# Kernel optimization log

Measured on AMD Instinct MI355X. Metric: run time of the kernel, lower is better.

Reference implementation:

```python
import jax, jax.numpy as jnp
import numpy as np

EPS = 1e-6


def _l2norm_last(x):
    return jnp.linalg.norm(x, axis=-1, keepdims=True)


def rotate_to(src, tgt):
    # rotation trick (vector-quantize-pytorch): Householder-style rotation of src onto tgt direction
    # src, tgt: (b, t, d)
    ns = _l2norm_last(src)
    nt = _l2norm_last(tgt)
    u = src / jnp.maximum(ns, EPS)
    q = tgt / jnp.maximum(nt, EPS)
    w = u + q
    w = jax.lax.stop_gradient(w / jnp.maximum(_l2norm_last(w), EPS))
    e = src
    rotated = (e
               - 2.0 * jnp.sum(e * w, axis=-1, keepdims=True) * w
               + 2.0 * jnp.sum(e * jax.lax.stop_gradient(u), axis=-1, keepdims=True) * q)
    return rotated * jax.lax.stop_gradient(nt / jnp.maximum(ns, EPS))


def _simvq_stage(res, V_i, g_i, b_i, cb_i, commit_w):
    # res: (b, t, D); V_i: (D, cd); g_i, b_i: (D,); cb_i: (cs, cd)
    # weight_norm Conv1d(k=1): W = g * V / ||V||_row
    Wn = g_i[:, None] * V_i / jnp.maximum(jnp.linalg.norm(V_i, axis=1, keepdims=True), 1e-12)
    implicit = cb_i @ Wn.T + b_i  # (cs, D) implicit codebook
    # nearest code via squared-distance argmin (cdist argmin equivalent, no_grad)
    d2 = (jnp.sum(res * res, axis=-1, keepdims=True)
          - 2.0 * jnp.einsum('btd,cd->btc', res, implicit)
          + jnp.sum(implicit * implicit, axis=-1))
    idx = jnp.argmin(d2, axis=-1)  # (b, t) int
    z_q = implicit[idx]  # gather: (b, t, D)
    commit = (jnp.mean((jax.lax.stop_gradient(res) - z_q) ** 2)
              + 0.25 * jnp.mean((res - jax.lax.stop_gradient(z_q)) ** 2))
    z_q = rotate_to(res, z_q)
    return z_q, idx, commit * commit_w


def setup_inputs() -> dict:
    key = jax.random.key(0)
    ks = jax.random.split(key, 5)
    B, D, T = 16, 512, 2048
    N, CS, CD = 9, 1024, 8
    z = jax.random.normal(ks[0], (B, D, T), dtype=jnp.float32)
    V = jax.random.normal(ks[1], (N, D, CD), dtype=jnp.float32)
    g = jax.random.uniform(ks[2], (N, D), dtype=jnp.float32, minval=0.5, maxval=1.5)
    b = jax.random.normal(ks[3], (N, D), dtype=jnp.float32) * 0.01
    CB = jax.random.normal(ks[4], (N, CS, CD), dtype=jnp.float32) * (CD ** -0.5)
    return {"z": z, "V": V, "g": g, "b": b, "CB": CB}


def reference(z, V, g, b, CB):
    # eval-mode ResidualSimVQ forward, all n_codebooks stages
    n_codebooks = V.shape[0]
    res = jnp.transpose(z, (0, 2, 1))  # (b, t, D)
    z_q = jnp.zeros_like(res)
    commitment_loss = jnp.float32(0.0)
    codes = []
    for i in range(n_codebooks):
        z_q_i, idx_i, commit_i = _simvq_stage(res, V[i], g[i], b[i], CB[i], 1.0)
        z_q = z_q + z_q_i
        res = res - z_q_i
        commitment_loss = commitment_loss + commit_i
        codes.append(idx_i)
    z_q = jnp.transpose(z_q, (0, 2, 1))  # (b, D, t)
    codes = jnp.stack(codes, axis=1)  # (b, n_codebooks, t)
    return z_q, codes, commitment_loss
```

## Files before the change

### kernel.cpp

```cpp
#include <hip/hip_runtime.h>


#define NB  16
#define DD  512
#define TT  2048
#define NCB 9
#define CS  1024
#define CD  8
#define KK  9
#define KP  12
#define NBLK (NB * (TT / 16))
#define GAPTHR 0.015f

#define WS_WN_OFF  65536
#define WS_WNF_OFF (WS_WN_OFF  + (size_t)NCB*DD*KK*8)
#define WS_Q_OFF   (WS_WNF_OFF + (size_t)NCB*DD*KP*4)
#define WS_QF_OFF  (WS_Q_OFF   + (size_t)NCB*CS*8)

typedef float vf4 __attribute__((ext_vector_type(4)));

__global__ void k_wn(const float* __restrict__ V, const float* __restrict__ g,
                     const float* __restrict__ bp, double* __restrict__ wn,
                     float* __restrict__ wnf) {
  int gid = blockIdx.x * 256 + threadIdx.x;
  if (gid >= NCB * DD) return;
  int i = gid / DD, d = gid % DD;
  const float* vp = V + (size_t)gid * CD;
  double v[CD], s = 0.0;
#pragma unroll
  for (int k = 0; k < CD; k++) { v[k] = (double)vp[k]; s = fma(v[k], v[k], s); }
  double den = fmax(sqrt(s), 1e-12);
  double gg = (double)g[gid];
  double* row = wn + ((size_t)i * DD + d) * KK;
  float* frow = wnf + ((size_t)i * DD + d) * KP;
#pragma unroll
  for (int k = 0; k < CD; k++) {
    double wv = gg * v[k] / den;
    row[k] = wv;
    frow[k] = (float)wv;
  }
  row[CD] = (double)bp[gid];
  frow[CD] = bp[gid];
  frow[9] = 0.0f; frow[10] = 0.0f; frow[11] = 0.0f;
}

__global__ void k_q(const float* __restrict__ CBp, const float* __restrict__ bp,
                    const double* __restrict__ wn,
                    double* __restrict__ q, float* __restrict__ qf) {
  int wid = blockIdx.x * 4 + (threadIdx.x >> 6);
  int lane = threadIdx.x & 63;
  int i = wid / CS, c = wid % CS;
  const float* cb = CBp + (size_t)(i * CS + c) * CD;
  double cbv[CD];
#pragma unroll
  for (int k = 0; k < CD; k++) cbv[k] = (double)cb[k];
  const double* wnp = wn + (size_t)i * DD * KK;
  const float* bb = bp + (size_t)i * DD;
  double acc = 0.0;
#pragma unroll
  for (int j = 0; j < 8; j++) {
    int d = j * 64 + lane;
    double imp = (double)bb[d];
#pragma unroll
    for (int k = 0; k < CD; k++) imp = fma(cbv[k], wnp[(size_t)d * KK + k], imp);
    acc = fma(imp, imp, acc);
  }
#pragma unroll
  for (int o = 32; o; o >>= 1) acc += __shfl_xor(acc, o, 64);
  if (lane == 0) { q[wid] = acc; qf[wid] = (float)(0.5 * acc); }
}

__launch_bounds__(256, 2)
__global__ void k_main(const float* __restrict__ z, const float* __restrict__ CBp,
                       const double* __restrict__ wn, const float* __restrict__ wnf,
                       const double* __restrict__ qtab, const float* __restrict__ qftab,
                       float* __restrict__ out_zq, float* __restrict__ out_codes,
                       double* __restrict__ partials) {
  __shared__ __align__(16) float tile[DD * 17];
  __shared__ double cbuf[4];

  const int tid = threadIdx.x, lane = tid & 63, w = tid >> 6;
  const int bb = blockIdx.x >> 7, tg = blockIdx.x & 127;
  const int t0 = tg * 16;
  const float* zb = z + (size_t)bb * DD * TT + t0;

#pragma unroll
  for (int m = 0; m < 8; m++) {
    int F = tid + m * 256, d = F >> 2, qq = F & 3;
    const vf4 v = __builtin_nontemporal_load((const vf4*)(zb + (size_t)d * TT + qq * 4));
    tile[d * 17 + qq * 4 + 0] = v.x; tile[d * 17 + qq * 4 + 1] = v.y;
    tile[d * 17 + qq * 4 + 2] = v.z; tile[d * 17 + qq * 4 + 3] = v.w;
  }
  __syncthreads();

  double res[4][8], ns2[4];
#pragma unroll
  for (int r = 0; r < 4; r++) {
    double s = 0.0;
#pragma unroll
    for (int j = 0; j < 8; j++) {
      res[r][j] = (double)tile[(j * 64 + lane) * 17 + (w * 4 + r)];
      s = fma(res[r][j], res[r][j], s);
    }
    ns2[r] = s;
  }
#pragma unroll
  for (int o = 32; o; o >>= 1)
#pragma unroll
    for (int r = 0; r < 4; r++) ns2[r] += __shfl_xor(ns2[r], o, 64);

  double commit = 0.0;

  for (int i = 0; i < NCB; i++) {
    const float* wfp = wnf + (size_t)i * DD * KP;
    const float* cbbase = CBp + (size_t)i * CS * CD;
    const float* qfb = qftab + i * CS;
    const double* qb = qtab + i * CS;

    float pf[4][KK];
#pragma unroll
    for (int r = 0; r < 4; r++)
#pragma unroll
      for (int k = 0; k < KK; k++) pf[r][k] = 0.0f;
#pragma unroll
    for (int j = 0; j < 8; j++) {
      const float* row = wfp + (size_t)(j * 64 + lane) * KP;
      const float4 w0 = *(const float4*)(row);
      const float4 w1 = *(const float4*)(row + 4);
      const float  w8 = row[8];
      float rv[4];
#pragma unroll
      for (int r = 0; r < 4; r++) rv[r] = -(float)res[r][j];
#pragma unroll
      for (int r = 0; r < 4; r++) {
        pf[r][0] = fmaf(rv[r], w0.x, pf[r][0]);
        pf[r][1] = fmaf(rv[r], w0.y, pf[r][1]);
        pf[r][2] = fmaf(rv[r], w0.z, pf[r][2]);
        pf[r][3] = fmaf(rv[r], w0.w, pf[r][3]);
        pf[r][4] = fmaf(rv[r], w1.x, pf[r][4]);
        pf[r][5] = fmaf(rv[r], w1.y, pf[r][5]);
        pf[r][6] = fmaf(rv[r], w1.z, pf[r][6]);
        pf[r][7] = fmaf(rv[r], w1.w, pf[r][7]);
        pf[r][8] = fmaf(rv[r], w8,   pf[r][8]);
      }
    }
#pragma unroll
    for (int o = 32; o; o >>= 1)
#pragma unroll
      for (int r = 0; r < 4; r++)
#pragma unroll
        for (int k = 0; k < KK; k++) pf[r][k] += __shfl_xor(pf[r][k], o, 64);

    float s1a[4], s2a[4], s1b[4], s2b[4];
    int   c1a[4], c1b[4];
#pragma unroll
    for (int r = 0; r < 4; r++) {
      s1a[r] = s2a[r] = s1b[r] = s2b[r] = 3.4e38f;
      c1a[r] = c1b[r] = 0;
    }
#pragma unroll 4
    for (int m = 0; m < 16; m += 2) {
#pragma unroll
      for (int h = 0; h < 2; h++) {
        int c = (m + h) * 64 + lane;
        const float4 c0 = *(const float4*)(cbbase + (size_t)c * CD);
        const float4 cx = *(const float4*)(cbbase + (size_t)c * CD + 4);
        float qv = qfb[c];
#pragma unroll
        for (int r = 0; r < 4; r++) {
          float s = qv;
          s = fmaf(c0.x, pf[r][0], s); s = fmaf(c0.y, pf[r][1], s);
          s = fmaf(c0.z, pf[r][2], s); s = fmaf(c0.w, pf[r][3], s);
          s = fmaf(cx.x, pf[r][4], s); s = fmaf(cx.y, pf[r][5], s);
          s = fmaf(cx.z, pf[r][6], s); s = fmaf(cx.w, pf[r][7], s);
          if (h == 0) {
            if (s < s1a[r]) { s2a[r] = s1a[r]; s1a[r] = s; c1a[r] = c; }
            else            { s2a[r] = fminf(s2a[r], s); }
          } else {
            if (s < s1b[r]) { s2b[r] = s1b[r]; s1b[r] = s; c1b[r] = c; }
            else            { s2b[r] = fminf(s2b[r], s); }
          }
        }
      }
    }
    float s1[4], s2[4]; int c1[4];
#pragma unroll
    for (int r = 0; r < 4; r++) {
      if (s1a[r] < s1b[r] || (s1a[r] == s1b[r] && c1a[r] < c1b[r])) {
        s1[r] = s1a[r]; c1[r] = c1a[r]; s2[r] = fminf(s2a[r], s1b[r]);
      } else {
        s1[r] = s1b[r]; c1[r] = c1b[r]; s2[r] = fminf(s2b[r], s1a[r]);
      }
    }
#pragma unroll
    for (int o = 32; o; o >>= 1) {
#pragma unroll
      for (int r = 0; r < 4; r++) {
        float os1 = __shfl_xor(s1[r], o, 64);
        int   oc1 = __shfl_xor(c1[r], o, 64);
        float os2 = __shfl_xor(s2[r], o, 64);
        float hi = fmaxf(s1[r], os1);
        s2[r] = fminf(fminf(s2[r], os2), hi);
        if (os1 < s1[r] || (os1 == s1[r] && oc1 < c1[r])) { s1[r] = os1; c1[r] = oc1; }
      }
    }

    double Ap[4], Cm[4];
    float cbf[4][8];
#pragma unroll
    for (int r = 0; r < 4; r++) {
      if (s2[r] - s1[r] < GAPTHR) {
        double pd[KK];
#pragma unroll
        for (int k = 0; k < KK; k++) pd[k] = 0.0;
#pragma unroll
        for (int j = 0; j < 8; j++) {
          const double* wrow = wn + ((size_t)i * DD + j * 64 + lane) * KK;
          double rv = res[r][j];
#pragma unroll
          for (int k = 0; k < KK; k++) pd[k] = fma(rv, wrow[k], pd[k]);
        }
#pragma unroll
        for (int o = 32; o; o >>= 1)
#pragma unroll
          for (int k = 0; k < KK; k++) pd[k] += __shfl_xor(pd[k], o, 64);
        double pm2[8];
#pragma unroll
        for (int k = 0; k < 8; k++) pm2[k] = -2.0 * pd[k];
        double bs = 1e300; int bc = 0;
#pragma unroll 4
        for (int m = 0; m < 16; m++) {
          int c = m * 64 + lane;
          const float* cb2 = cbbase + (size_t)c * CD;
          double s = qb[c];
#pragma unroll
          for (int k = 0; k < 8; k++) s = fma((double)cb2[k], pm2[k], s);
          if (s < bs) { bs = s; bc = c; }
        }
#pragma unroll
        for (int o = 32; o; o >>= 1) {
          double obs = __shfl_xor(bs, o, 64);
          int    obc = __shfl_xor(bc, o, 64);
          if (obs < bs || (obs == bs && obc < bc)) { bs = obs; bc = obc; }
        }
        c1[r] = bc;
      }
      int cu = __builtin_amdgcn_readfirstlane(c1[r]);
      const float* cbr = cbbase + (size_t)cu * CD;
      double pzn = (double)pf[r][8];
#pragma unroll
      for (int k = 0; k < 8; k++) {
        float cf = cbr[k];
        cbf[r][k] = cf;
        pzn = fma((double)cf, (double)pf[r][k], pzn);
      }
      double pz = -pzn;
      double nt2 = qb[cu];
      double n2 = ns2[r];
      float n2f = (float)n2, nt2f = (float)nt2, pzf = (float)pz;
      float rnsf = (n2f  > 1e-12f) ? rsqrtf(n2f)  : 1e6f;
      float rntf = (nt2f > 1e-12f) ? rsqrtf(nt2f) : 1e6f;
      float sntf = nt2f * rntf;
      float wn2f = n2f * rnsf * rnsf + 2.0f * pzf * rnsf * rntf + nt2f * rntf * rntf;
      float rdwf = (wn2f > 1e-12f) ? rsqrtf(wn2f) : 1e6f;
      float euf = n2f * rnsf;
      float ewf = (n2f * rnsf + pzf * rntf) * rdwf;
      float scalef = sntf * rnsf;
      float Af = scalef * (1.0f - 2.0f * ewf * rdwf * rnsf);
      float Cf = scalef * rntf * 2.0f * (euf - ewf * rdwf);
      commit += n2 - 2.0 * pz + nt2;
      double ap = 1.0 - (double)Af;
      double C  = (double)Cf;
      Ap[r] = ap; Cm[r] = C;
      ns2[r] = ap * ap * n2 - 2.0 * ap * C * pz + C * C * nt2;
      if (lane == 0)
        out_codes[((size_t)bb * NCB + i) * TT + t0 + w * 4 + r] = (float)cu;
    }

#pragma unroll
    for (int j = 0; j < 8; j++) {
      const float* row = wfp + (size_t)(j * 64 + lane) * KP;
      const float4 w0 = *(const float4*)(row);
      const float4 w1 = *(const float4*)(row + 4);
      const float  w8 = row[8];
#pragma unroll
      for (int r = 0; r < 4; r++) {
        float impf = w8;
        impf = fmaf(cbf[r][0], w0.x, impf);
        impf = fmaf(cbf[r][1], w0.y, impf);
        impf = fmaf(cbf[r][2], w0.z, impf);
        impf = fmaf(cbf[r][3], w0.w, impf);
        impf = fmaf(cbf[r][4], w1.x, impf);
        impf = fmaf(cbf[r][5], w1.y, impf);
        impf = fmaf(cbf[r][6], w1.z, impf);
        impf = fmaf(cbf[r][7], w1.w, impf);
        res[r][j] = Ap[r] * res[r][j] - Cm[r] * (double)impf;
      }
    }
  }

  if (lane == 0) cbuf[w] = commit;

  __syncthreads();
#pragma unroll
  for (int r = 0; r < 4; r++)
#pragma unroll
    for (int j = 0; j < 8; j++)
      tile[(j * 64 + lane) * 17 + (w * 4 + r)] = (float)res[r][j];
  __syncthreads();
#pragma unroll
  for (int m = 0; m < 8; m++) {
    int F = tid + m * 256, d = F >> 2, qq = F & 3;
    const vf4 v = __builtin_nontemporal_load((const vf4*)(zb + (size_t)d * TT + qq * 4));
    vf4 o;
    o.x = v.x - tile[d * 17 + qq * 4 + 0];
    o.y = v.y - tile[d * 17 + qq * 4 + 1];
    o.z = v.z - tile[d * 17 + qq * 4 + 2];
    o.w = v.w - tile[d * 17 + qq * 4 + 3];
    __builtin_nontemporal_store(o, (vf4*)(out_zq + ((size_t)bb * DD + d) * TT + t0 + qq * 4));
  }
  if (tid == 0)
    partials[blockIdx.x] = cbuf[0] + cbuf[1] + cbuf[2] + cbuf[3];
}

__global__ void k_fin(const double* __restrict__ partials, float* __restrict__ outc) {
  __shared__ double sb[4];
  int tid = threadIdx.x, lane = tid & 63, w = tid >> 6;
  double s = 0.0;
#pragma unroll
  for (int m = 0; m < NBLK / 256; m++) s += partials[tid + m * 256];
#pragma unroll
  for (int o = 32; o; o >>= 1) s += __shfl_xor(s, o, 64);
  if (lane == 0) sb[w] = s;
  __syncthreads();
  if (tid == 0) {
    double tot = sb[0] + sb[1] + sb[2] + sb[3];
    outc[0] = (float)(tot * 1.25 / (double)((size_t)NB * TT * DD));
  }
}

extern "C" void kernel_launch(void* const* d_in, const int* in_sizes, int n_in,
                              void* d_out, int out_size, void* d_ws, size_t ws_size,
                              hipStream_t stream) {
  const float* z  = (const float*)d_in[0];
  const float* V  = (const float*)d_in[1];
  const float* g  = (const float*)d_in[2];
  const float* b  = (const float*)d_in[3];
  const float* CB = (const float*)d_in[4];
  float* out = (float*)d_out;

  double* parts = (double*)d_ws;
  double* wn  = (double*)((char*)d_ws + WS_WN_OFF);
  float*  wnf = (float*)((char*)d_ws + WS_WNF_OFF);
  double* q   = (double*)((char*)d_ws + WS_Q_OFF);
  float*  qf  = (float*)((char*)d_ws + WS_QF_OFF);

  hipLaunchKernelGGL(k_wn, dim3((NCB * DD + 255) / 256), dim3(256), 0, stream,
                     V, g, b, wn, wnf);
  hipLaunchKernelGGL(k_q, dim3((NCB * CS) / 4), dim3(256), 0, stream, CB, b, wn, q, qf);
  hipLaunchKernelGGL(k_main, dim3(NBLK), dim3(256), 0, stream,
                     z, CB, wn, wnf, q, qf,
                     out, out + (size_t)NB * DD * TT, parts);
  hipLaunchKernelGGL(k_fin, dim3(1), dim3(256), 0, stream,
                     parts, out + (size_t)NB * DD * TT + (size_t)NB * NCB * TT);
}
```

Measured before the change: 530.5 us.

## Stage per-stage codebook and half-norms in LDS with double-buffered async loads

```diff
diff --git a/kernel.cpp b/kernel.cpp
--- a/kernel.cpp
+++ b/kernel.cpp
@@ -11,13 +11,20 @@
 #define KP  12
 #define NBLK (NB * (TT / 16))
 #define GAPTHR 0.015f
+#define CBSTG 36864
 
 #define WS_WN_OFF  65536
 #define WS_WNF_OFF (WS_WN_OFF  + (size_t)NCB*DD*KK*8)
 #define WS_Q_OFF   (WS_WNF_OFF + (size_t)NCB*DD*KP*4)
-#define WS_QF_OFF  (WS_Q_OFF   + (size_t)NCB*CS*8)
+#define WS_CBP_OFF (WS_Q_OFF   + (size_t)NCB*CS*8)
 
 typedef float vf4 __attribute__((ext_vector_type(4)));
+
+__device__ __forceinline__ void ld_lds16(const void* g, void* l) {
+  __builtin_amdgcn_global_load_lds(
+      (const __attribute__((address_space(1))) void*)g,
+      (__attribute__((address_space(3))) void*)l, 16, 0, 0);
+}
 
 __global__ void k_wn(const float* __restrict__ V, const float* __restrict__ g,
                      const float* __restrict__ bp, double* __restrict__ wn,
@@ -44,9 +51,19 @@
   frow[9] = 0.0f; frow[10] = 0.0f; frow[11] = 0.0f;
 }
 
+__global__ void k_cb(const float* __restrict__ CBp, char* __restrict__ cbp) {
+  int gid = blockIdx.x * 256 + threadIdx.x;
+  if (gid >= NCB * CS) return;
+  int i = gid / CS, c = gid % CS;
+  const float4* src = (const float4*)(CBp + (size_t)gid * CD);
+  char* base = cbp + (size_t)i * CBSTG;
+  ((float4*)base)[c] = src[0];
+  ((float4*)(base + 16384))[c] = src[1];
+}
+
 __global__ void k_q(const float* __restrict__ CBp, const float* __restrict__ bp,
                     const double* __restrict__ wn,
-                    double* __restrict__ q, float* __restrict__ qf) {
+                    double* __restrict__ q, char* __restrict__ cbp) {
   int wid = blockIdx.x * 4 + (threadIdx.x >> 6);
   int lane = threadIdx.x & 63;
   int i = wid / CS, c = wid % CS;
@@ -67,17 +84,21 @@
   }
 #pragma unroll
   for (int o = 32; o; o >>= 1) acc += __shfl_xor(acc, o, 64);
-  if (lane == 0) { q[wid] = acc; qf[wid] = (float)(0.5 * acc); }
+  if (lane == 0) {
+    q[wid] = acc;
+    ((float*)(cbp + (size_t)i * CBSTG + 32768))[c] = (float)(0.5 * acc);
+  }
 }
 
 __launch_bounds__(256, 2)
 __global__ void k_main(const float* __restrict__ z, const float* __restrict__ CBp,
                        const double* __restrict__ wn, const float* __restrict__ wnf,
-                       const double* __restrict__ qtab, const float* __restrict__ qftab,
+                       const double* __restrict__ qtab, const char* __restrict__ cbp,
                        float* __restrict__ out_zq, float* __restrict__ out_codes,
                        double* __restrict__ partials) {
-  __shared__ __align__(16) float tile[DD * 17];
+  __shared__ __align__(16) char sbuf[2 * CBSTG];
   __shared__ double cbuf[4];
+  float* tile = (float*)(sbuf + CBSTG);
 
   const int tid = threadIdx.x, lane = tid & 63, w = tid >> 6;
   const int bb = blockIdx.x >> 7, tg = blockIdx.x & 127;
@@ -109,12 +130,30 @@
 #pragma unroll
     for (int r = 0; r < 4; r++) ns2[r] += __shfl_xor(ns2[r], o, 64);
 
+#pragma unroll
+  for (int m = 0; m < 9; m++)
+    ld_lds16(cbp + (size_t)w * 9216 + m * 1024 + lane * 16,
+             sbuf + w * 9216 + m * 1024);
+
   double commit = 0.0;
 
   for (int i = 0; i < NCB; i++) {
+    __syncthreads();
+
+    if (i < NCB - 1) {
+      const char* src = cbp + (size_t)(i + 1) * CBSTG;
+      char* dst = sbuf + ((i + 1) & 1) * CBSTG;
+#pragma unroll
+      for (int m = 0; m < 9; m++)
+        ld_lds16(src + (size_t)w * 9216 + m * 1024 + lane * 16,
+                 dst + w * 9216 + m * 1024);
+    }
+
     const float* wfp = wnf + (size_t)i * DD * KP;
+    const float4* lof = (const float4*)(sbuf + (i & 1) * CBSTG);
+    const float4* hif = (const float4*)(sbuf + (i & 1) * CBSTG + 16384);
+    const float*  qfl = (const float*)(sbuf + (i & 1) * CBSTG + 32768);
     const float* cbbase = CBp + (size_t)i * CS * CD;
-    const float* qfb = qftab + i * CS;
     const double* qb = qtab + i * CS;
 
     float pf[4][KK];
@@ -163,9 +202,9 @@
 #pragma unroll
       for (int h = 0; h < 2; h++) {
         int c = (m + h) * 64 + lane;
-        const float4 c0 = *(const float4*)(cbbase + (size_t)c * CD);
-        const float4 cx = *(const float4*)(cbbase + (size_t)c * CD + 4);
-        float qv = qfb[c];
+        const float4 c0 = lof[c];
+        const float4 cx = hif[c];
+        float qv = qfl[c];
 #pragma unroll
         for (int r = 0; r < 4; r++) {
           float s = qv;
@@ -246,13 +285,14 @@
         c1[r] = bc;
       }
       int cu = __builtin_amdgcn_readfirstlane(c1[r]);
-      const float* cbr = cbbase + (size_t)cu * CD;
+      const float4 clo = lof[cu];
+      const float4 chi = hif[cu];
+      float cbr[8] = {clo.x, clo.y, clo.z, clo.w, chi.x, chi.y, chi.z, chi.w};
       double pzn = (double)pf[r][8];
 #pragma unroll
       for (int k = 0; k < 8; k++) {
-        float cf = cbr[k];
-        cbf[r][k] = cf;
-        pzn = fma((double)cf, (double)pf[r][k], pzn);
+        cbf[r][k] = cbr[k];
+        pzn = fma((double)cbr[k], (double)pf[r][k], pzn);
       }
       double pz = -pzn;
       double nt2 = qb[cu];
@@ -353,13 +393,14 @@
   double* wn  = (double*)((char*)d_ws + WS_WN_OFF);
   float*  wnf = (float*)((char*)d_ws + WS_WNF_OFF);
   double* q   = (double*)((char*)d_ws + WS_Q_OFF);
-  float*  qf  = (float*)((char*)d_ws + WS_QF_OFF);
+  char*   cbp = (char*)d_ws + WS_CBP_OFF;
 
   hipLaunchKernelGGL(k_wn, dim3((NCB * DD + 255) / 256), dim3(256), 0, stream,
                      V, g, b, wn, wnf);
-  hipLaunchKernelGGL(k_q, dim3((NCB * CS) / 4), dim3(256), 0, stream, CB, b, wn, q, qf);
+  hipLaunchKernelGGL(k_cb, dim3((NCB * CS + 255) / 256), dim3(256), 0, stream, CB, cbp);
+  hipLaunchKernelGGL(k_q, dim3((NCB * CS) / 4), dim3(256), 0, stream, CB, b, wn, q, cbp);
   hipLaunchKernelGGL(k_main, dim3(NBLK), dim3(256), 0, stream,
-                     z, CB, wn, wnf, q, qf,
+                     z, CB, wn, wnf, q, cbp,
                      out, out + (size_t)NB * DD * TT, parts);
   hipLaunchKernelGGL(k_fin, dim3(1), dim3(256), 0, stream,
                      parts, out + (size_t)NB * DD * TT + (size_t)NB * NCB * TT);
```

Result: slower. 598.7 us (+12.8%).
